# Kernel optimization log

Measured on AMD Instinct MI355X. Metric: run time of the kernel, lower is better.

## Reference

```python
import jax, jax.numpy as jnp
import numpy as np

B, N, C, D, K, H, A = 4, 2048, 128, 128, 16, 64, 512


def _rn(k, shape, s):
    return (jax.random.normal(k, shape) * s).astype(jnp.float32)


def setup_inputs():
    ks = jax.random.split(jax.random.key(0), 40)
    w = lambda i, o, c: _rn(ks[i], (o, c), 0.02)
    b = lambda i, o: _rn(ks[i + 20], (o,), 0.02)
    p = {}
    p["xyz"] = _rn(ks[0], (B, 3, N), 1.0)
    p["pos"] = _rn(ks[1], (B, 2, N), 1.0)
    p["key"] = _rn(ks[2], (B, C, N), 1.0)
    p["query"] = _rn(ks[3], (B, C, N), 1.0)
    p["mv_w1"] = w(4, C, 2 * C); p["mv_b1"] = b(4, C)
    p["mv_w2"] = w(5, C, C);     p["mv_b2"] = b(5, C)
    p["mv_ws"] = w(6, C, 2 * C); p["mv_bs"] = b(6, C)
    p["wk"] = w(7, D, C); p["bk"] = b(7, D)
    p["wq"] = w(8, D, C); p["bq"] = b(8, D)
    p["wv"] = w(9, D, C); p["bv"] = b(9, D)
    p["xyz_w1"] = w(10, H, 3); p["xyz_b1"] = b(10, H)
    p["xyz_w2"] = w(11, D, H); p["xyz_b2"] = b(11, D)
    p["pos_w1"] = w(12, H, 2); p["pos_b1"] = b(12, H)
    p["pos_w2"] = w(13, D, H); p["pos_b2"] = b(13, D)
    p["xat_w1"] = w(14, A, D); p["xat_b1"] = b(14, A)
    p["xat_w2"] = w(15, D, A); p["xat_b2"] = b(15, D)
    p["at_w1"] = w(16, A, D); p["at_b1"] = b(16, A)
    p["at_w2"] = w(17, D, A); p["at_b2"] = b(17, D)
    p["wkq"] = w(18, C, D); p["bkq"] = b(18, C)
    p["wend"] = w(19, C, D); p["bend"] = b(19, C)
    return p


def c1(w, b, x):  # 1x1 Conv1d: (O,C) on (B,C,N)
    return jnp.einsum('oc,bcn->bon', w, x) + b[None, :, None]


def c2(w, b, x):  # 1x1 Conv2d: (O,C) on (B,C,N,K)
    return jnp.einsum('oc,bcnk->bonk', w, x) + b[None, :, None, None]


def mlp2(w1, b1, w2, b2, x):
    return c2(w2, b2, jax.nn.relu(c2(w1, b1, x)))


def softmax_one(x):  # exp(x-m) / (1 + sum exp(x-m)) over last axis
    m = jnp.max(x, axis=-1, keepdims=True)
    e = jnp.exp(x - m)
    return e / (1.0 + jnp.sum(e, axis=-1, keepdims=True))


def knn_idx(pts, k):  # pts: (B, N, d) -> (B, N, k) indices, include_self=True
    sq = jnp.sum(pts * pts, axis=-1)
    d2 = sq[:, :, None] + sq[:, None, :] - 2.0 * jnp.einsum('bnd,bmd->bnm', pts, pts)
    return jnp.argsort(d2, axis=-1)[:, :, :k]


def group(f, idx):  # f: (B,C,N), idx: (B,N,K) -> (B,C,N,K)
    return jax.vmap(lambda a, i: a[:, i])(f, idx)


def reference(xyz, pos, key, query, mv_w1, mv_b1, mv_w2, mv_b2, mv_ws, mv_bs,
              wk, bk, wq, bq, wv, bv, xyz_w1, xyz_b1, xyz_w2, xyz_b2,
              pos_w1, pos_b1, pos_w2, pos_b2, xat_w1, xat_b1, xat_w2, xat_b2,
              at_w1, at_b1, at_w2, at_b2, wkq, bkq, wend, bend):
    cat = jnp.concatenate([key, query], axis=1)  # (B, 2C, N)
    # MLP_Res
    value = c1(mv_w2, mv_b2, jax.nn.relu(c1(mv_w1, mv_b1, cat))) + c1(mv_ws, mv_bs, cat)
    identity = value
    k = c1(wk, bk, key)
    q = c1(wq, bq, query)
    v = c1(wv, bv, value)
    # ---- block 1: xyz-space kNN attention ----
    idx1 = knn_idx(jnp.swapaxes(xyz, 1, 2), K)           # (B,N,K)
    kq_rel = k[..., None] - group(q, idx1)               # (B,D,N,K)
    xyz_rel = xyz[..., None] - group(xyz, idx1)          # (B,3,N,K)
    xyz_emb = mlp2(xyz_w1, xyz_b1, xyz_w2, xyz_b2, xyz_rel)
    xa = softmax_one(mlp2(xat_w1, xat_b1, xat_w2, xat_b2, kq_rel + xyz_emb))
    agg = jnp.sum(xa * (v[..., None] + xyz_emb), axis=-1)  # (B,D,N)
    value = c1(wkq, bkq, agg) + identity
    value = c1(wv, bv, value)
    # ---- block 2: pos-space kNN attention ----
    idx2 = knn_idx(jnp.swapaxes(pos, 1, 2), K)
    qk_rel = q[..., None] - group(k, idx2)
    pos_rel = pos[..., None] - group(pos, idx2)
    pos_emb = mlp2(pos_w1, pos_b1, pos_w2, pos_b2, pos_rel)
    at = softmax_one(mlp2(at_w1, at_b1, at_w2, at_b2, qk_rel + pos_emb))
    agg = jnp.sum(at * (value[..., None] + pos_emb), axis=-1)
    y = c1(wend, bend, agg)
    return y + identity
```

## Files before the change

kernel.cpp:

```cpp
#include <hip/hip_runtime.h>
#include <hip/hip_bf16.h>

typedef __hip_bfloat16 bf16;
typedef unsigned long long ull;

#define BB 4
#define NN 2048
#define CCH 128
#define DDM 128
#define KNB 16
#define HHD 64
#define AAD 512
#define PP (BB*NN)

typedef __attribute__((ext_vector_type(8))) short short8;
typedef __attribute__((ext_vector_type(16))) float f32x16;

__device__ __forceinline__ float b2f(bf16 x) { return __bfloat162float(x); }
__device__ __forceinline__ bf16 f2b(float x) { return __float2bfloat16(x); }

__device__ __forceinline__ float ldany(const void* p, size_t i, int f32) {
  return f32 ? ((const float*)p)[i] : __bfloat162float(((const bf16*)p)[i]);
}

__device__ __forceinline__ long pack4(float a, float b, float c, float d) {
  union { bf16 h[4]; long l; } u;
  u.h[0] = f2b(a); u.h[1] = f2b(b); u.h[2] = f2b(c); u.h[3] = f2b(d);
  return u.l;
}
__device__ __forceinline__ void unpack4(long l, float* o) {
  union { bf16 h[4]; long l; } u; u.l = l;
  o[0] = b2f(u.h[0]); o[1] = b2f(u.h[1]); o[2] = b2f(u.h[2]); o[3] = b2f(u.h[3]);
}

__device__ __forceinline__ short8 ldfrag(const bf16* base, int row, int stride, int k0, int hl) {
  const bf16* p = base + (size_t)row * stride + k0 + (hl << 3);
  union { short8 v; long l[2]; } u;
  u.l[0] = *(const long*)p;
  u.l[1] = *(const long*)(p + 4);
  return u.v;
}

__device__ __forceinline__ f32x16 MFMA(short8 a, short8 b, f32x16 c) {
  return __builtin_amdgcn_mfma_f32_32x32x16_bf16(a, b, c, 0, 0, 0);
}

struct PtrArr { const void* p[36]; int n[36]; };
struct CvtTab { int src[16]; int off[16]; int n[16]; int isb[16]; };
struct G4 { const bf16* X[4]; int K[4]; int woff[4]; int boff[4]; bf16* out[4]; int relu[4]; };

__global__ __launch_bounds__(256) void sniff_kern(PtrArr pa, int* __restrict__ flags) {
  int t = blockIdx.x;
  const bf16* x = (const bf16*)pa.p[t];
  int n = pa.n[t]; if (n > 4096) n = 4096;
  __shared__ int cnt;
  if (threadIdx.x == 0) cnt = 0;
  __syncthreads();
  int c = 0;
  for (int i = threadIdx.x; i < n; i += 256) {
    float v = fabsf(__bfloat162float(x[i]));
    if (v == 0.f || (v >= 1e-6f && v <= 1024.f)) c++;
  }
  atomicAdd(&cnt, c);
  __syncthreads();
  if (threadIdx.x == 0) flags[t] = (cnt >= (n * 7) / 8) ? 0 : 1;
}

__global__ __launch_bounds__(256) void prep_all_kern(PtrArr pa, CvtTab tab,
                                                     const int* __restrict__ flags,
                                                     bf16* __restrict__ warena, float* __restrict__ barena,
                                                     bf16* __restrict__ w1img0, bf16* __restrict__ w2img0,
                                                     bf16* __restrict__ cw2img0, float* __restrict__ fb0,
                                                     bf16* __restrict__ w1img1, bf16* __restrict__ w2img1,
                                                     bf16* __restrict__ cw2img1, float* __restrict__ fb1,
                                                     const void* __restrict__ keyp, const void* __restrict__ qryp,
                                                     const void* __restrict__ xyzp, const void* __restrict__ posp,
                                                     bf16* __restrict__ catT,
                                                     float* __restrict__ xyzT, float* __restrict__ posT) {
  int y = blockIdx.y;
  int tid = threadIdx.x;
  int bx = blockIdx.x;
  if (y == 18) {
    if (bx >= 512) return;
    __shared__ float tile[64][65];
    int xx = bx & 31, yy = (bx >> 5) & 1, zz = bx >> 6;
    int b = zz & 3, half = zz >> 2;
    const void* src = half ? qryp : keyp;
    const int f32 = flags[2 + half];
    int n0 = xx * 64, c0 = yy * 64;
    int tx = tid & 63, ty = tid >> 6;
    for (int r = ty; r < 64; r += 4)
      tile[r][tx] = ldany(src, (size_t)(b * 128 + c0 + r) * NN + n0 + tx, f32);
    __syncthreads();
    for (int r = ty; r < 64; r += 4)
      catT[(size_t)(b * NN + n0 + r) * 256 + half * 128 + c0 + tx] = __float2bfloat16(tile[tx][r]);
    return;
  }
  if (y == 19) {
    if (bx >= 256) return;
    int which = bx >> 7;
    const void* src = which ? posp : xyzp;
    float* dst = which ? posT : xyzT;
    int dd = which ? 2 : 3;
    const int f32 = flags[which];
    int i = (bx & 127) * 256 * 2 + tid;
    for (int rep = 0; rep < 2; ++rep, i += 256) {
      if (i < PP * 4) {
        int p = i >> 2, j = i & 3;
        int b = p >> 11, n = p & (NN - 1);
        dst[i] = (j < dd) ? ldany(src, (size_t)(b * dd + j) * NN + n, f32) : 0.f;
      }
    }
    return;
  }
  if (y >= 2) {
    int e = y - 2;
    int i = bx * 256 + tid;
    if (i >= tab.n[e]) return;
    float v = ldany(pa.p[tab.src[e]], i, flags[tab.src[e]]);
    if (tab.isb[e]) barena[tab.off[e] + i] = v;
    else warena[tab.off[e] + i] = f2b(v);
    return;
  }
  int set = y;
  int cIdx = set ? 20 : 16, aIdx = set ? 28 : 24, dd = set ? 2 : 3;
  bf16* w1img = set ? w1img1 : w1img0;
  bf16* w2img = set ? w2img1 : w2img0;
  bf16* cw2img = set ? cw2img1 : cw2img0;
  float* fb = set ? fb1 : fb0;
  const void* cw1 = pa.p[cIdx];     const void* cb1 = pa.p[cIdx + 1];
  const void* cw2 = pa.p[cIdx + 2]; const void* cb2 = pa.p[cIdx + 3];
  const void* aw1 = pa.p[aIdx];     const void* ab1 = pa.p[aIdx + 1];
  const void* aw2 = pa.p[aIdx + 2]; const void* ab2 = pa.p[aIdx + 3];
  int i = bx * 256 + tid;
  const int fcw1 = flags[cIdx], fcb1 = flags[cIdx + 1];
  const int fcw2 = flags[cIdx + 2], fcb2 = flags[cIdx + 3];
  const int faw1 = flags[aIdx], fab1 = flags[aIdx + 1];
  const int faw2 = flags[aIdx + 2], fab2 = flags[aIdx + 3];
  float* ab1f = fb;
  float* ab2f = fb + 512;
  float* cb1f = fb + 640;
  float* cb2f = fb + 704;
  float* cw1f = fb + 832;
  if (i < 65536) {
    int hg = i >> 7, c = i & 127;
    w1img[(size_t)hg * 132 + c] = f2b(ldany(aw1, i, faw1));
  } else if (i < 131072) {
    int j = i - 65536;
    int o = j >> 9, hh = j & 511;
    int ac = hh >> 7, hloc = hh & 127;
    w2img[(size_t)(ac * 128 + o) * 132 + hloc] = f2b(ldany(aw2, j, faw2));
  } else if (i < 139264) {
    int j = i - 131072;
    int o = j >> 6, h = j & 63;
    cw2img[o * 68 + h] = f2b(ldany(cw2, j, fcw2));
  } else if (i < 139776) {
    int j = i - 139264; ab1f[j] = ldany(ab1, j, fab1);
  } else if (i < 139904) {
    int j = i - 139776; ab2f[j] = ldany(ab2, j, fab2);
  } else if (i < 139968) {
    int j = i - 139904; cb1f[j] = ldany(cb1, j, fcb1);
  } else if (i < 140096) {
    int j = i - 139968; cb2f[j] = ldany(cb2, j, fcb2);
  } else if (i < 140288) {
    int j = i - 140096;
    int h = j / 3, c = j % 3;
    cw1f[j] = (c < dd) ? ldany(cw1, h * dd + c, fcw1) : 0.f;
  }
}

__global__ __launch_bounds__(512) void mega_kern(
    const float* __restrict__ xyzT, const float* __restrict__ posT,
    int* __restrict__ idx1, int* __restrict__ idx2,
    G4 g, bf16* __restrict__ warena, float* __restrict__ barena) {
  __shared__ __attribute__((aligned(16))) char smem[33280];
  int bx = blockIdx.x;
  int tid = threadIdx.x, lane = tid & 63, wvv = tid >> 6;
  if (bx < 2048) {
    float4* cds = (float4*)smem;
    int set = bx >> 10;
    int pblk = bx & 1023;
    const float* coordsT = set ? posT : xyzT;
    int* idxout = set ? idx2 : idx1;
    int p0 = pblk * 8, b = p0 >> 11;
    for (int j = tid; j < NN; j += 512)
      cds[j] = *(const float4*)&coordsT[((size_t)(b << 11) + j) * 4];
    __syncthreads();
    int p = p0 + wvv, n = p & (NN - 1);
    float4 cc = cds[n];
    float sqi = __fadd_rn(__fadd_rn(__fmul_rn(cc.x, cc.x), __fmul_rn(cc.y, cc.y)),
                          __fmul_rn(cc.z, cc.z));
    ull t[32];
#pragma unroll
    for (int s = 0; s < 32; ++s) {
      int j = (s << 6) | lane;
      float4 q = cds[j];
      float sqj = __fadd_rn(__fadd_rn(__fmul_rn(q.x, q.x), __fmul_rn(q.y, q.y)),
                            __fmul_rn(q.z, q.z));
      float dt  = __fadd_rn(__fadd_rn(__fmul_rn(cc.x, q.x), __fmul_rn(cc.y, q.y)),
                            __fmul_rn(cc.z, q.z));
      float d2 = __fsub_rn(__fadd_rn(sqi, sqj), __fmul_rn(2.f, dt));
      unsigned u = __float_as_uint(d2);
      u = (u & 0x80000000u) ? ~u : (u | 0x80000000u);
      t[s] = ((ull)u << 32) | (unsigned)j;
    }
#pragma unroll
    for (int base = 0; base < 32; base += 16) {
#pragma unroll
      for (int k = 2; k <= 16; k <<= 1) {
#pragma unroll
        for (int j = k >> 1; j > 0; j >>= 1) {
#pragma unroll
          for (int i = 0; i < 16; ++i) {
            int l = i ^ j;
            if (l > i) {
              bool up = ((i & k) == 0);
              ull a = t[base + i], c = t[base + l];
              ull lo = a < c ? a : c;
              ull hi = a < c ? c : a;
              t[base + i] = up ? lo : hi;
              t[base + l] = up ? hi : lo;
            }
          }
        }
      }
    }
#pragma unroll
    for (int i = 0; i < 16; ++i) {
      ull a = t[i], c = t[31 - i];
      t[i] = a < c ? a : c;
    }
#pragma unroll
    for (int j = 8; j > 0; j >>= 1) {
#pragma unroll
      for (int i = 0; i < 16; ++i) {
        int l = i ^ j;
        if (l > i) {
          ull a = t[i], c = t[l];
          ull lo = a < c ? a : c;
          ull hi = a < c ? c : a;
          t[i] = lo; t[l] = hi;
        }
      }
    }
    for (int r = 0; r < KNB; ++r) {
      ull h = t[0];
      ull m = h;
#pragma unroll
      for (int off = 1; off < 64; off <<= 1) {
        ull o = __shfl_xor(m, off);
        m = o < m ? o : m;
      }
      if (lane == 0) idxout[(size_t)p * KNB + r] = (int)(m & 0xffffffffu);
      if (h == m) {
#pragma unroll
        for (int i = 0; i < 15; ++i) t[i] = t[i + 1];
        t[15] = ~0ull;
      }
    }
    return;
  }
  if (bx < 2560) {
    bf16* XT = (bf16*)smem;
    int bx2 = bx - 2048;
    int op = bx2 >> 7, ptile = bx2 & 127;
    const bf16* X = g.X[op];
    int K = g.K[op];
    const bf16* Wb = warena + g.woff[op];
    const float* bias = barena + g.boff[op];
    bf16* out = g.out[op];
    int relu = g.relu[op];
    int hl = lane >> 5, cA = lane & 31;
    int p0 = ptile * 64;
    int SK = K + 4;
    int kc = K >> 3;
    for (int c = tid; c < 64 * kc; c += 512) {
      int r = c / kc, col = (c % kc) << 3;
      *(float4*)&XT[r * SK + col] = *(const float4*)&X[(size_t)(p0 + r) * 256 + col];
    }
    __syncthreads();
    int o0 = (wvv & 3) * 32;
    int tt = wvv >> 2;
    f32x16 acc;
#pragma unroll
    for (int r = 0; r < 16; ++r) {
      int o = o0 + (r & 3) + 8 * (r >> 2) + 4 * hl;
      acc[r] = bias[o];
    }
    for (int ks = 0; ks < (K >> 4); ++ks) {
      short8 af = ldfrag(Wb, o0 + cA, K, ks * 16, hl);
      short8 b0 = ldfrag(XT, tt * 32 + cA, SK, ks * 16, hl);
      acc = MFMA(af, b0, acc);
    }
    int m = p0 + tt * 32 + cA;
#pragma unroll
    for (int q = 0; q < 4; ++q) {
      int ob = o0 + 8 * q + 4 * hl;
      float v[4] = {acc[4*q+0], acc[4*q+1], acc[4*q+2], acc[4*q+3]};
      if (relu) {
        v[0] = fmaxf(v[0], 0.f); v[1] = fmaxf(v[1], 0.f);
        v[2] = fmaxf(v[2], 0.f); v[3] = fmaxf(v[3], 0.f);
      }
      *(long*)(out + (size_t)m * 128 + ob) = pack4(v[0], v[1], v[2], v[3]);
    }
    return;
  }
  {
    bf16* WT = (bf16*)smem;
    const bf16* wvw = warena + 114688;
    const bf16* wkq = warena + 131072;
    for (int i = tid; i < 16384; i += 512) {
      int k = i >> 7, j = i & 127;
      WT[j * 128 + k] = wkq[k * 128 + j];
    }
    __syncthreads();
    int hl = lane >> 5, cA = lane & 31;
    int istrip = (wvv & 3) * 32;
    int jt0 = (wvv >> 2) * 64;
#pragma unroll
    for (int t = 0; t < 2; ++t) {
      f32x16 acc;
#pragma unroll
      for (int r = 0; r < 16; ++r) acc[r] = 0.f;
#pragma unroll
      for (int ks = 0; ks < 8; ++ks) {
        short8 af = ldfrag(wvw, istrip + cA, 128, ks * 16, hl);
        short8 b0 = ldfrag(WT, jt0 + t * 32 + cA, 128, ks * 16, hl);
        acc = MFMA(af, b0, acc);
      }
      int j = jt0 + t * 32 + cA;
#pragma unroll
      for (int r = 0; r < 16; ++r) {
        int i_ = istrip + (r & 3) + 8 * (r >> 2) + 4 * hl;
        warena[163840 + i_ * 128 + j] = f2b(acc[r]);
      }
    }
    if (tid < 128) {
      float acc = 0.f;
      const float* bkq = barena + 768;
      for (int k = 0; k < 128; ++k)
        acc += b2f(wvw[tid * 128 + k]) * bkq[k];
      barena[1024 + tid] = acc;
    }
  }
}

#define SMEM_BYTES 72192
__global__ __launch_bounds__(512, 4) void attn_mfma(
    const bf16* __restrict__ centerT, const bf16* __restrict__ gatherT,
    const float* __restrict__ coordsT, const bf16* __restrict__ vfeatT,
    const int* __restrict__ idx,
    const bf16* __restrict__ w1img, const bf16* __restrict__ w2img,
    const bf16* __restrict__ cw2img, const float* __restrict__ fb,
    const bf16* __restrict__ wout, const float* __restrict__ bout,
    const bf16* __restrict__ residG, void* __restrict__ outAny, int outMode,
    const int* __restrict__ flags,
    const bf16* __restrict__ sFp, const bf16* __restrict__ sGp,
    const bf16* __restrict__ mvw2, const float* __restrict__ mvb2,
    const bf16* __restrict__ wvw, const float* __restrict__ bvf,
    bf16* __restrict__ v0out, int fuseChain) {
  extern __shared__ char smem[];
  bf16* XS  = (bf16*)(smem);
  bf16* HT  = (bf16*)(smem + 33792);
  bf16* HC  = HT;
  bf16* CFE = (bf16*)(smem + 67584);
  bf16* VF  = (bf16*)(smem + 69632);
  int*  NID = (int*)(smem + 71680);
  const float* ab1f = fb;
  const float* ab2f = fb + 512;
  const float* cb1f = fb + 640;
  const float* cb2f = fb + 704;
  const float* cw1f = fb + 832;

  int tid = threadIdx.x, lane = tid & 63, wv = tid >> 6;
  int hl = lane >> 5, cA = lane & 31;
  int P0 = blockIdx.x * 8, b = P0 >> 11;

  if (tid < 128) NID[tid] = (b << 11) + idx[(size_t)(P0 + (tid >> 4)) * KNB + (tid & 15)];
  if (fuseChain) {
    for (int i = tid; i < 1024; i += 512) {
      int g = i >> 7, d = i & 127;
      CFE[i] = centerT[(size_t)(P0 + g) * 128 + d];
      XS[g * 132 + d] = sFp[(size_t)(P0 + g) * 128 + d];
      XS[(8 + g) * 132 + d] = sGp[(size_t)(P0 + g) * 128 + d];
    }
    __syncthreads();
    if (wv < 4) {
      int o0m = wv * 32;
      f32x16 a1;
#pragma unroll
      for (int r = 0; r < 16; ++r) {
        int o = o0m + (r & 3) + 8 * (r >> 2) + 4 * hl;
        a1[r] = mvb2[o];
      }
#pragma unroll
      for (int ks = 0; ks < 8; ++ks) {
        short8 af = ldfrag(mvw2, o0m + cA, 128, ks * 16, hl);
        short8 b0 = ldfrag(XS, cA, 132, ks * 16, hl);
        a1 = MFMA(af, b0, a1);
      }
      int m = cA;
      if (m < 8) {
#pragma unroll
        for (int q = 0; q < 4; ++q) {
          int ob = o0m + 8 * q + 4 * hl;
          float sg[4];
          unpack4(*(long*)&XS[(8 + m) * 132 + ob], sg);
          long pk = pack4(a1[4*q+0] + sg[0], a1[4*q+1] + sg[1],
                          a1[4*q+2] + sg[2], a1[4*q+3] + sg[3]);
          *(long*)&HT[m * 132 + ob] = pk;
          *(long*)(v0out + (size_t)(P0 + m) * 128 + ob) = pk;
        }
      }
    }
    __syncthreads();
    if (wv < 4) {
      int o0m = wv * 32;
      f32x16 a2;
#pragma unroll
      for (int r = 0; r < 16; ++r) {
        int o = o0m + (r & 3) + 8 * (r >> 2) + 4 * hl;
        a2[r] = bvf[o];
      }
#pragma unroll
      for (int ks = 0; ks < 8; ++ks) {
        short8 af = ldfrag(wvw, o0m + cA, 128, ks * 16, hl);
        short8 b0 = ldfrag(HT, cA, 132, ks * 16, hl);
        a2 = MFMA(af, b0, a2);
      }
      int m = cA;
      if (m < 8) {
#pragma unroll
        for (int q = 0; q < 4; ++q) {
          int ob = o0m + 8 * q + 4 * hl;
          *(long*)&VF[m * 128 + ob] = pack4(a2[4*q+0], a2[4*q+1], a2[4*q+2], a2[4*q+3]);
        }
      }
    }
    __syncthreads();
  } else {
    for (int i = tid; i < 1024; i += 512) {
      int g = i >> 7, d = i & 127;
      CFE[i] = centerT[(size_t)(P0 + g) * 128 + d];
      VF[i]  = vfeatT[(size_t)(P0 + g) * 128 + d];
    }
    __syncthreads();
  }

  {
    int m = tid >> 2, sub = tid & 3;
    float4 ccd = *(const float4*)&coordsT[(size_t)(P0 + (m >> 4)) * 4];
    float4 nbd = *(const float4*)&coordsT[(size_t)NID[m] * 4];
    float r0 = ccd.x - nbd.x, r1 = ccd.y - nbd.y, r2 = ccd.z - nbd.z;
    int h0 = sub * 16;
    for (int hh = h0; hh < h0 + 16; hh += 4) {
      float a0 = fmaxf(cb1f[hh+0] + cw1f[(hh+0)*3]*r0 + cw1f[(hh+0)*3+1]*r1 + cw1f[(hh+0)*3+2]*r2, 0.f);
      float a1 = fmaxf(cb1f[hh+1] + cw1f[(hh+1)*3]*r0 + cw1f[(hh+1)*3+1]*r1 + cw1f[(hh+1)*3+2]*r2, 0.f);
      float a2 = fmaxf(cb1f[hh+2] + cw1f[(hh+2)*3]*r0 + cw1f[(hh+2)*3+1]*r1 + cw1f[(hh+2)*3+2]*r2, 0.f);
      float a3 = fmaxf(cb1f[hh+3] + cw1f[(hh+3)*3]*r0 + cw1f[(hh+3)*3+1]*r1 + cw1f[(hh+3)*3+2]*r2, 0.f);
      *(long*)&HC[m * 68 + hh] = pack4(a0, a1, a2, a3);
    }
    const bf16* grow = gatherT + (size_t)NID[m] * 128 + sub * 32;
    const bf16* crow = CFE + ((m >> 4) << 7) + sub * 32;
    for (int j = 0; j < 32; j += 4) {
      float gv[4], cv[4];
      unpack4(*(const long*)(grow + j), gv);
      unpack4(*(const long*)(crow + j), cv);
      *(long*)&XS[m * 132 + sub * 32 + j] =
          pack4(cv[0] - gv[0], cv[1] - gv[1], cv[2] - gv[2], cv[3] - gv[3]);
    }
  }
  __syncthreads();

  int r0s = (wv & 3) * 32;
  int mt0 = (wv >> 2) * 64;

  short8 pf[8];
#pragma unroll
  for (int ks = 0; ks < 8; ++ks)
    pf[ks] = ldfrag(w1img, r0s + cA, 132, ks * 16, hl);

  {
    f32x16 eacc[2];
#pragma unroll
    for (int r = 0; r < 16; ++r) {
      int o = r0s + (r & 3) + 8 * (r >> 2) + 4 * hl;
      float bv = cb2f[o];
      eacc[0][r] = bv; eacc[1][r] = bv;
    }
    for (int k0 = 0; k0 < 64; k0 += 16) {
      short8 af = ldfrag(cw2img, r0s + cA, 68, k0, hl);
      short8 b0 = ldfrag(HC, mt0 + cA, 68, k0, hl);
      short8 b1 = ldfrag(HC, mt0 + 32 + cA, 68, k0, hl);
      eacc[0] = MFMA(af, b0, eacc[0]);
      eacc[1] = MFMA(af, b1, eacc[1]);
    }
#pragma unroll
    for (int t = 0; t < 2; ++t) {
      int m = mt0 + t * 32 + cA;
#pragma unroll
      for (int q = 0; q < 4; ++q) {
        int ob = r0s + 8 * q + 4 * hl;
        bf16* px = &XS[m * 132 + ob];
        float xv[4];
        unpack4(*(long*)px, xv);
        *(long*)px = pack4(xv[0] + eacc[t][4*q+0], xv[1] + eacc[t][4*q+1],
                           xv[2] + eacc[t][4*q+2], xv[3] + eacc[t][4*q+3]);
      }
    }
  }
  __syncthreads();

  f32x16 acc2[2];
#pragma unroll
  for (int r = 0; r < 16; ++r) {
    int o = r0s + (r & 3) + 8 * (r >> 2) + 4 * hl;
    float bv = ab2f[o];
    acc2[0][r] = bv; acc2[1][r] = bv;
  }

  for (int ac = 0; ac < 4; ++ac) {
    const bf16* w2c = w2img + (size_t)ac * 16896;
    const bf16* w1n = w1img + (size_t)((ac + 1) & 3) * 16896;
    f32x16 acc1[2];
#pragma unroll
    for (int r = 0; r < 16; ++r) {
      int h = r0s + (r & 3) + 8 * (r >> 2) + 4 * hl;
      float bv = ab1f[ac * 128 + h];
      acc1[0][r] = bv; acc1[1][r] = bv;
    }
#pragma unroll
    for (int ks = 0; ks < 8; ++ks) {
      short8 af = pf[ks];
      short8 b0 = ldfrag(XS, mt0 + cA, 132, ks * 16, hl);
      short8 b1 = ldfrag(XS, mt0 + 32 + cA, 132, ks * 16, hl);
      pf[ks] = ldfrag(w2c, r0s + cA, 132, ks * 16, hl);
      acc1[0] = MFMA(af, b0, acc1[0]);
      acc1[1] = MFMA(af, b1, acc1[1]);
    }
    __syncthreads();
#pragma unroll
    for (int t = 0; t < 2; ++t) {
      int m = mt0 + t * 32 + cA;
#pragma unroll
      for (int q = 0; q < 4; ++q) {
        int hb = r0s + 8 * q + 4 * hl;
        *(long*)&HT[m * 132 + hb] =
            pack4(fmaxf(acc1[t][4*q+0], 0.f), fmaxf(acc1[t][4*q+1], 0.f),
                  fmaxf(acc1[t][4*q+2], 0.f), fmaxf(acc1[t][4*q+3], 0.f));
      }
    }
    __syncthreads();
#pragma unroll
    for (int ks = 0; ks < 8; ++ks) {
      short8 af = pf[ks];
      short8 b0 = ldfrag(HT, mt0 + cA, 132, ks * 16, hl);
      short8 b1 = ldfrag(HT, mt0 + 32 + cA, 132, ks * 16, hl);
      pf[ks] = ldfrag(w1n, r0s + cA, 132, ks * 16, hl);
      acc2[0] = MFMA(af, b0, acc2[0]);
      acc2[1] = MFMA(af, b1, acc2[1]);
    }
  }

  __syncthreads();
#pragma unroll
  for (int t = 0; t < 2; ++t) {
    int m = mt0 + t * 32 + cA;
#pragma unroll
    for (int q = 0; q < 4; ++q) {
      int ob = r0s + 8 * q + 4 * hl;
      *(long*)&HT[m * 132 + ob] = pack4(acc2[t][4*q+0], acc2[t][4*q+1],
                                        acc2[t][4*q+2], acc2[t][4*q+3]);
    }
  }
  __syncthreads();

  float agg0, agg1v;
  {
    int g = wv;
    int base = g * 16;
    float vbase0 = b2f(VF[g * 128 + lane])      - b2f(CFE[g * 128 + lane]);
    float vbase1 = b2f(VF[g * 128 + lane + 64]) - b2f(CFE[g * 128 + lane + 64]);
#pragma unroll
    for (int half = 0; half < 2; ++half) {
      int o = lane + half * 64;
      float vb = half ? vbase1 : vbase0;
      float e[16];
      float mx = -3.4e38f;
#pragma unroll
      for (int kk = 0; kk < 16; ++kk) {
        float x = b2f(HT[(base + kk) * 132 + o]);
        e[kk] = x;
        mx = fmaxf(mx, x);
      }
      float s = 0.f;
#pragma unroll
      for (int kk = 0; kk < 16; ++kk) { e[kk] = __expf(e[kk] - mx); s += e[kk]; }
      float inv = 1.f / (1.f + s);
      float acc = 0.f;
#pragma unroll
      for (int kk = 0; kk < 16; ++kk) {
        float xv = b2f(XS[(base + kk) * 132 + o]);
        float gv = b2f(gatherT[(size_t)NID[base + kk] * 128 + o]);
        acc += (e[kk] * inv) * (vb + xv + gv);
      }
      if (half) agg1v = acc; else agg0 = acc;
    }
  }
  __syncthreads();
  {
    int g = wv;
    HT[g * 132 + lane] = f2b(agg0);
    HT[g * 132 + lane + 64] = f2b(agg1v);
  }
  __syncthreads();

  float* XSf = (float*)XS;
  if (wv < 4) {
    int o0m = wv * 32;
    f32x16 acc;
#pragma unroll
    for (int r = 0; r < 16; ++r) {
      int o = o0m + (r & 3) + 8 * (r >> 2) + 4 * hl;
      acc[r] = bout[o];
    }
#pragma unroll
    for (int ks = 0; ks < 8; ++ks) {
      short8 af = ldfrag(wout, o0m + cA, 128, ks * 16, hl);
      short8 b0 = ldfrag(HT, cA, 132, ks * 16, hl);
      acc = MFMA(af, b0, acc);
    }
    int m = cA;
    if (m < 8) {
      int gp = P0 + m;
#pragma unroll
      for (int q = 0; q < 4; ++q) {
        int ob = o0m + 8 * q + 4 * hl;
        float rv[4];
        if (outMode) unpack4(*(const long*)(residG + (size_t)gp * 128 + ob), rv);
        else         unpack4(*(long*)&VF[m * 128 + ob], rv);
        float v0o = acc[4*q+0] + rv[0];
        float v1o = acc[4*q+1] + rv[1];
        float v2o = acc[4*q+2] + rv[2];
        float v3o = acc[4*q+3] + rv[3];
        if (outMode) {
          float4 st = {v0o, v1o, v2o, v3o};
          *(float4*)&XSf[m * 128 + ob] = st;
        } else {
          *(long*)((bf16*)outAny + (size_t)gp * 128 + ob) = pack4(v0o, v1o, v2o, v3o);
        }
      }
    }
  }
  if (outMode) {
    __syncthreads();
    if (tid < 128) {
      int c = tid;
      int gb = P0 >> 11, gn0 = P0 & (NN - 1);
      if (flags[2]) {
        float* op = (float*)outAny + (size_t)(gb * 128 + c) * NN + gn0;
        float4 v0v, v1v;
        v0v.x = XSf[0 * 128 + c]; v0v.y = XSf[1 * 128 + c];
        v0v.z = XSf[2 * 128 + c]; v0v.w = XSf[3 * 128 + c];
        v1v.x = XSf[4 * 128 + c]; v1v.y = XSf[5 * 128 + c];
        v1v.z = XSf[6 * 128 + c]; v1v.w = XSf[7 * 128 + c];
        *(float4*)op = v0v;
        *(float4*)(op + 4) = v1v;
      } else {
        bf16* op = (bf16*)outAny + (size_t)(gb * 128 + c) * NN + gn0;
        long l0 = pack4(XSf[0 * 128 + c], XSf[1 * 128 + c], XSf[2 * 128 + c], XSf[3 * 128 + c]);
        long l1 = pack4(XSf[4 * 128 + c], XSf[5 * 128 + c], XSf[6 * 128 + c], XSf[7 * 128 + c]);
        *(long*)op = l0;
        *(long*)(op + 4) = l1;
      }
    }
  }
}

extern "C" void kernel_launch(void* const* d_in, const int* in_sizes, int n_in,
                              void* d_out, int out_size, void* d_ws, size_t ws_size,
                              hipStream_t stream) {
  int* flags = (int*)d_ws;
  bf16* catT = (bf16*)((float*)d_ws + 64);
  bf16* v0   = catT + (size_t)PP * 256;
  bf16* kT   = v0 + (size_t)PP * 128;
  bf16* qT   = kT + (size_t)PP * 128;
  bf16* sE   = qT + (size_t)PP * 128;
  bf16* sF   = sE + (size_t)PP * 128;
  bf16* sG   = sF + (size_t)PP * 128;
  float* xyzT = (float*)(sG + (size_t)PP * 128);
  float* posT = xyzT + (size_t)PP * 4;
  int* idx1 = (int*)(posT + (size_t)PP * 4);
  int* idx2 = idx1 + (size_t)PP * KNB;
  bf16* w1i1 = (bf16*)(idx2 + (size_t)PP * KNB);
  bf16* w2i1 = w1i1 + 67584;
  bf16* cw2i1 = w2i1 + 67584;
  bf16* w1i2 = cw2i1 + 8704;
  bf16* w2i2 = w1i2 + 67584;
  bf16* cw2i2 = w2i2 + 67584;
  float* fb1 = (float*)(cw2i2 + 8704);
  float* fb2 = fb1 + 1024;
  bf16* warena = (bf16*)(fb2 + 1024);
  float* barena = (float*)(warena + 180224);

  PtrArr pa;
  for (int i = 0; i < 36; ++i) { pa.p[i] = d_in[i]; pa.n[i] = in_sizes[i]; }
  sniff_kern<<<dim3(36), 256, 0, stream>>>(pa, flags);

  CvtTab tab;
  int wsrc[8] = {4, 8, 6, 10, 12, 14, 32, 34};
  int woff[8] = {0, 32768, 65536, 81920, 98304, 114688, 131072, 147456};
  int wn[8]   = {32768, 32768, 16384, 16384, 16384, 16384, 16384, 16384};
  int bsrc[8] = {5, 9, 7, 11, 13, 15, 33, 35};
  for (int e = 0; e < 8; ++e) {
    tab.src[e] = wsrc[e]; tab.off[e] = woff[e]; tab.n[e] = wn[e]; tab.isb[e] = 0;
    tab.src[8 + e] = bsrc[e]; tab.off[8 + e] = e * 128; tab.n[8 + e] = 128; tab.isb[8 + e] = 1;
  }
  prep_all_kern<<<dim3(548, 20), 256, 0, stream>>>(pa, tab, flags, warena, barena,
                                                   w1i1, w2i1, cw2i1, fb1,
                                                   w1i2, w2i2, cw2i2, fb2,
                                                   d_in[2], d_in[3], d_in[0], d_in[1],
                                                   catT, xyzT, posT);

  G4 g4;
  g4.X[0] = catT;       g4.K[0] = 256; g4.woff[0] = 0;      g4.boff[0] = 0;   g4.out[0] = sF; g4.relu[0] = 1;
  g4.X[1] = catT;       g4.K[1] = 256; g4.woff[1] = 32768;  g4.boff[1] = 128; g4.out[1] = sG; g4.relu[1] = 0;
  g4.X[2] = catT;       g4.K[2] = 128; g4.woff[2] = 81920;  g4.boff[2] = 384; g4.out[2] = kT; g4.relu[2] = 0;
  g4.X[3] = catT + 128; g4.K[3] = 128; g4.woff[3] = 98304;  g4.boff[3] = 512; g4.out[3] = qT; g4.relu[3] = 0;
  mega_kern<<<dim3(2048 + 512 + 1), 512, 0, stream>>>(xyzT, posT, idx1, idx2, g4, warena, barena);

  hipFuncSetAttribute((const void*)attn_mfma, hipFuncAttributeMaxDynamicSharedMemorySize, SMEM_BYTES);

  attn_mfma<<<dim3(PP / 8), 512, SMEM_BYTES, stream>>>(kT, qT, xyzT, nullptr, idx1,
                                                       w1i1, w2i1, cw2i1, fb1,
                                                       warena + 163840, barena + 1024,
                                                       nullptr, sE, 0, flags,
                                                       sF, sG,
                                                       warena + 65536, barena + 256,
                                                       warena + 114688, barena + 640,
                                                       v0, 1);
  attn_mfma<<<dim3(PP / 8), 512, SMEM_BYTES, stream>>>(qT, kT, posT, sE, idx2,
                                                       w1i2, w2i2, cw2i2, fb2,
                                                       warena + 147456, barena + 896,
                                                       v0, d_out, 1, flags,
                                                       nullptr, nullptr,
                                                       nullptr, nullptr,
                                                       nullptr, nullptr,
                                                       nullptr, 0);
}
```

Baseline: 388.5 us.

## Move pos-space kNN into first attention launch to overlap with attention

```diff
diff --git a/kernel.cpp b/kernel.cpp
--- a/kernel.cpp
+++ b/kernel.cpp
@@ -48,6 +48,88 @@
 struct PtrArr { const void* p[36]; int n[36]; };
 struct CvtTab { int src[16]; int off[16]; int n[16]; int isb[16]; };
 struct G4 { const bf16* X[4]; int K[4]; int woff[4]; int boff[4]; bf16* out[4]; int relu[4]; };
+
+__device__ __forceinline__ void knn_block(const float* __restrict__ coordsT,
+                                          int* __restrict__ idxout,
+                                          int pblk, int tid, float4* cds) {
+  int lane = tid & 63, wvv = tid >> 6;
+  int p0 = pblk * 8, b = p0 >> 11;
+  for (int j = tid; j < NN; j += 512)
+    cds[j] = *(const float4*)&coordsT[((size_t)(b << 11) + j) * 4];
+  __syncthreads();
+  int p = p0 + wvv, n = p & (NN - 1);
+  float4 cc = cds[n];
+  float sqi = __fadd_rn(__fadd_rn(__fmul_rn(cc.x, cc.x), __fmul_rn(cc.y, cc.y)),
+                        __fmul_rn(cc.z, cc.z));
+  ull t[32];
+#pragma unroll
+  for (int s = 0; s < 32; ++s) {
+    int j = (s << 6) | lane;
+    float4 q = cds[j];
+    float sqj = __fadd_rn(__fadd_rn(__fmul_rn(q.x, q.x), __fmul_rn(q.y, q.y)),
+                          __fmul_rn(q.z, q.z));
+    float dt  = __fadd_rn(__fadd_rn(__fmul_rn(cc.x, q.x), __fmul_rn(cc.y, q.y)),
+                          __fmul_rn(cc.z, q.z));
+    float d2 = __fsub_rn(__fadd_rn(sqi, sqj), __fmul_rn(2.f, dt));
+    unsigned u = __float_as_uint(d2);
+    u = (u & 0x80000000u) ? ~u : (u | 0x80000000u);
+    t[s] = ((ull)u << 32) | (unsigned)j;
+  }
+#pragma unroll
+  for (int base = 0; base < 32; base += 16) {
+#pragma unroll
+    for (int k = 2; k <= 16; k <<= 1) {
+#pragma unroll
+      for (int j = k >> 1; j > 0; j >>= 1) {
+#pragma unroll
+        for (int i = 0; i < 16; ++i) {
+          int l = i ^ j;
+          if (l > i) {
+            bool up = ((i & k) == 0);
+            ull a = t[base + i], c = t[base + l];
+            ull lo = a < c ? a : c;
+            ull hi = a < c ? c : a;
+            t[base + i] = up ? lo : hi;
+            t[base + l] = up ? hi : lo;
+          }
+        }
+      }
+    }
+  }
+#pragma unroll
+  for (int i = 0; i < 16; ++i) {
+    ull a = t[i], c = t[31 - i];
+    t[i] = a < c ? a : c;
+  }
+#pragma unroll
+  for (int j = 8; j > 0; j >>= 1) {
+#pragma unroll
+    for (int i = 0; i < 16; ++i) {
+      int l = i ^ j;
+      if (l > i) {
+        ull a = t[i], c = t[l];
+        ull lo = a < c ? a : c;
+        ull hi = a < c ? c : a;
+        t[i] = lo; t[l] = hi;
+      }
+    }
+  }
+  for (int r = 0; r < KNB; ++r) {
+    ull h = t[0];
+    ull m = h;
+#pragma unroll
+    for (int off = 1; off < 64; off <<= 1) {
+      ull o = __shfl_xor(m, off);
+      m = o < m ? o : m;
+    }
+    if (lane == 0) idxout[(size_t)p * KNB + r] = (int)(m & 0xffffffffu);
+    if (h == m) {
+#pragma unroll
+      for (int i = 0; i < 15; ++i) t[i] = t[i + 1];
+      t[15] = ~0ull;
+    }
+  }
+}
 
 __global__ __launch_bounds__(256) void sniff_kern(PtrArr pa, int* __restrict__ flags) {
   int t = blockIdx.x;
@@ -170,99 +252,19 @@
 }
 
 __global__ __launch_bounds__(512) void mega_kern(
-    const float* __restrict__ xyzT, const float* __restrict__ posT,
-    int* __restrict__ idx1, int* __restrict__ idx2,
+    const float* __restrict__ xyzT,
+    int* __restrict__ idx1,
     G4 g, bf16* __restrict__ warena, float* __restrict__ barena) {
   __shared__ __attribute__((aligned(16))) char smem[33280];
   int bx = blockIdx.x;
   int tid = threadIdx.x, lane = tid & 63, wvv = tid >> 6;
-  if (bx < 2048) {
-    float4* cds = (float4*)smem;
-    int set = bx >> 10;
-    int pblk = bx & 1023;
-    const float* coordsT = set ? posT : xyzT;
-    int* idxout = set ? idx2 : idx1;
-    int p0 = pblk * 8, b = p0 >> 11;
-    for (int j = tid; j < NN; j += 512)
-      cds[j] = *(const float4*)&coordsT[((size_t)(b << 11) + j) * 4];
-    __syncthreads();
-    int p = p0 + wvv, n = p & (NN - 1);
-    float4 cc = cds[n];
-    float sqi = __fadd_rn(__fadd_rn(__fmul_rn(cc.x, cc.x), __fmul_rn(cc.y, cc.y)),
-                          __fmul_rn(cc.z, cc.z));
-    ull t[32];
-#pragma unroll
-    for (int s = 0; s < 32; ++s) {
-      int j = (s << 6) | lane;
-      float4 q = cds[j];
-      float sqj = __fadd_rn(__fadd_rn(__fmul_rn(q.x, q.x), __fmul_rn(q.y, q.y)),
-                            __fmul_rn(q.z, q.z));
-      float dt  = __fadd_rn(__fadd_rn(__fmul_rn(cc.x, q.x), __fmul_rn(cc.y, q.y)),
-                            __fmul_rn(cc.z, q.z));
-      float d2 = __fsub_rn(__fadd_rn(sqi, sqj), __fmul_rn(2.f, dt));
-      unsigned u = __float_as_uint(d2);
-      u = (u & 0x80000000u) ? ~u : (u | 0x80000000u);
-      t[s] = ((ull)u << 32) | (unsigned)j;
-    }
-#pragma unroll
-    for (int base = 0; base < 32; base += 16) {
-#pragma unroll
-      for (int k = 2; k <= 16; k <<= 1) {
-#pragma unroll
-        for (int j = k >> 1; j > 0; j >>= 1) {
-#pragma unroll
-          for (int i = 0; i < 16; ++i) {
-            int l = i ^ j;
-            if (l > i) {
-              bool up = ((i & k) == 0);
-              ull a = t[base + i], c = t[base + l];
-              ull lo = a < c ? a : c;
-              ull hi = a < c ? c : a;
-              t[base + i] = up ? lo : hi;
-              t[base + l] = up ? hi : lo;
-            }
-          }
-        }
-      }
-    }
-#pragma unroll
-    for (int i = 0; i < 16; ++i) {
-      ull a = t[i], c = t[31 - i];
-      t[i] = a < c ? a : c;
-    }
-#pragma unroll
-    for (int j = 8; j > 0; j >>= 1) {
-#pragma unroll
-      for (int i = 0; i < 16; ++i) {
-        int l = i ^ j;
-        if (l > i) {
-          ull a = t[i], c = t[l];
-          ull lo = a < c ? a : c;
-          ull hi = a < c ? c : a;
-          t[i] = lo; t[l] = hi;
-        }
-      }
-    }
-    for (int r = 0; r < KNB; ++r) {
-      ull h = t[0];
-      ull m = h;
-#pragma unroll
-      for (int off = 1; off < 64; off <<= 1) {
-        ull o = __shfl_xor(m, off);
-        m = o < m ? o : m;
-      }
-      if (lane == 0) idxout[(size_t)p * KNB + r] = (int)(m & 0xffffffffu);
-      if (h == m) {
-#pragma unroll
-        for (int i = 0; i < 15; ++i) t[i] = t[i + 1];
-        t[15] = ~0ull;
-      }
-    }
+  if (bx < 1024) {
+    knn_block(xyzT, idx1, bx, tid, (float4*)smem);
     return;
   }
-  if (bx < 2560) {
+  if (bx < 1536) {
     bf16* XT = (bf16*)smem;
-    int bx2 = bx - 2048;
+    int bx2 = bx - 1024;
     int op = bx2 >> 7, ptile = bx2 & 127;
     const bf16* X = g.X[op];
     int K = g.K[op];
@@ -358,8 +360,15 @@
     const bf16* __restrict__ sFp, const bf16* __restrict__ sGp,
     const bf16* __restrict__ mvw2, const float* __restrict__ mvb2,
     const bf16* __restrict__ wvw, const float* __restrict__ bvf,
-    bf16* __restrict__ v0out, int fuseChain) {
+    bf16* __restrict__ v0out, int fuseChain,
+    const float* __restrict__ knnCoords, int* __restrict__ knnIdxOut, int nAttn) {
   extern __shared__ char smem[];
+  int tid = threadIdx.x;
+  int bxg = blockIdx.x;
+  if (bxg >= nAttn) {
+    knn_block(knnCoords, knnIdxOut, bxg - nAttn, tid, (float4*)smem);
+    return;
+  }
   bf16* XS  = (bf16*)(smem);
   bf16* HT  = (bf16*)(smem + 33792);
   bf16* HC  = HT;
@@ -372,9 +381,9 @@
   const float* cb2f = fb + 704;
   const float* cw1f = fb + 832;
 
-  int tid = threadIdx.x, lane = tid & 63, wv = tid >> 6;
+  int lane = tid & 63, wv = tid >> 6;
   int hl = lane >> 5, cA = lane & 31;
-  int P0 = blockIdx.x * 8, b = P0 >> 11;
+  int P0 = bxg * 8, b = P0 >> 11;
 
   if (tid < 128) NID[tid] = (b << 11) + idx[(size_t)(P0 + (tid >> 4)) * KNB + (tid & 15)];
   if (fuseChain) {
@@ -727,24 +736,28 @@
   g4.X[1] = catT;       g4.K[1] = 256; g4.woff[1] = 32768;  g4.boff[1] = 128; g4.out[1] = sG; g4.relu[1] = 0;
   g4.X[2] = catT;       g4.K[2] = 128; g4.woff[2] = 81920;  g4.boff[2] = 384; g4.out[2] = kT; g4.relu[2] = 0;
   g4.X[3] = catT + 128; g4.K[3] = 128; g4.woff[3] = 98304;  g4.boff[3] = 512; g4.out[3] = qT; g4.relu[3] = 0;
-  mega_kern<<<dim3(2048 + 512 + 1), 512, 0, stream>>>(xyzT, posT, idx1, idx2, g4, warena, barena);
+  mega_kern<<<dim3(1024 + 512 + 1), 512, 0, stream>>>(xyzT, idx1, g4, warena, barena);
 
   hipFuncSetAttribute((const void*)attn_mfma, hipFuncAttributeMaxDynamicSharedMemorySize, SMEM_BYTES);
 
-  attn_mfma<<<dim3(PP / 8), 512, SMEM_BYTES, stream>>>(kT, qT, xyzT, nullptr, idx1,
-                                                       w1i1, w2i1, cw2i1, fb1,
-                                                       warena + 163840, barena + 1024,
-                                                       nullptr, sE, 0, flags,
-                                                       sF, sG,
-                                                       warena + 65536, barena + 256,
-                                                       warena + 114688, barena + 640,
-                                                       v0, 1);
-  attn_mfma<<<dim3(PP / 8), 512, SMEM_BYTES, stream>>>(qT, kT, posT, sE, idx2,
-                                                       w1i2, w2i2, cw2i2, fb2,
-                                                       warena + 147456, barena + 896,
-                                                       v0, d_out, 1, flags,
-                                                       nullptr, nullptr,
-                                                       nullptr, nullptr,
-                                                       nullptr, nullptr,
-                                                       nullptr, 0);
-}
+  attn_mfma<<<dim3(PP / 8 + PP / 8), 512, SMEM_BYTES, stream>>>(
+      kT, qT, xyzT, nullptr, idx1,
+      w1i1, w2i1, cw2i1, fb1,
+      warena + 163840, barena + 1024,
+      nullptr, sE, 0, flags,
+      sF, sG,
+      warena + 65536, barena + 256,
+      warena + 114688, barena + 640,
+      v0, 1,
+      posT, idx2, PP / 8);
+  attn_mfma<<<dim3(PP / 8), 512, SMEM_BYTES, stream>>>(
+      qT, kT, posT, sE, idx2,
+      w1i2, w2i2, cw2i2, fb2,
+      warena + 147456, barena + 896,
+      v0, d_out, 1, flags,
+      nullptr, nullptr,
+      nullptr, nullptr,
+      nullptr, nullptr,
+      nullptr, 0,
+      nullptr, nullptr, PP / 8);
+}
```

Measured after the change: 393.6 us. Within noise of the previous version (+1.3%).
